# Optimization experiments

Measured on AMD Instinct MI355X. Metric: run time of the kernel, lower is better.

Reference implementation:

```python
import jax, jax.numpy as jnp
import numpy as np
import math

D_MODEL = 512
NHEAD = 8
HEAD_DIM = D_MODEL // NHEAD
LN_EPS = 1e-5


def _layernorm(x, g, b):
    mu = jnp.mean(x, axis=-1, keepdims=True)
    var = jnp.mean(jnp.square(x - mu), axis=-1, keepdims=True)
    return (x - mu) * jax.lax.rsqrt(var + LN_EPS) * g + b


def setup_inputs() -> dict:
    key = jax.random.key(0)
    ks = jax.random.split(key, 12)
    B, N, D = 4, 2048, D_MODEL
    s = 1.0 / math.sqrt(D)
    inp = {
        "hidden": jax.random.normal(ks[0], (B, N, D), jnp.float32),
        "adjacency": (jax.random.uniform(ks[1], (B, N, N)) > 0.98).astype(jnp.float32),
        "Wq": jax.random.normal(ks[2], (D, D), jnp.float32) * s,
        "bq": jnp.zeros((D,), jnp.float32),
        "Wk": jax.random.normal(ks[3], (D, D), jnp.float32) * s,
        "bk": jnp.zeros((D,), jnp.float32),
        "Wv": jax.random.normal(ks[4], (D, D), jnp.float32) * s,
        "bv": jnp.zeros((D,), jnp.float32),
        "Wo": jax.random.normal(ks[5], (D, D), jnp.float32) * s,
        "bo": jnp.zeros((D,), jnp.float32),
        "g1": jnp.ones((D,), jnp.float32),
        "b1": jnp.zeros((D,), jnp.float32),
        "g2": jnp.ones((D,), jnp.float32),
        "b2": jnp.zeros((D,), jnp.float32),
        "Wf1": jax.random.normal(ks[6], (D, 4 * D), jnp.float32) * s,
        "bf1": jnp.zeros((4 * D,), jnp.float32),
        "Wf2": jax.random.normal(ks[7], (4 * D, D), jnp.float32) * (1.0 / math.sqrt(4 * D)),
        "bf2": jnp.zeros((D,), jnp.float32),
    }
    return inp


def reference(hidden, adjacency, Wq, bq, Wk, bk, Wv, bv, Wo, bo,
              g1, b1, g2, b2, Wf1, bf1, Wf2, bf2):
    B, N, D = hidden.shape
    H, Hd = NHEAD, HEAD_DIM
    normed = _layernorm(hidden, g1, b1)
    # projections -> [B, H, N, Hd]
    q = (normed @ Wq + bq).reshape(B, N, H, Hd).transpose(0, 2, 1, 3)
    k = (normed @ Wk + bk).reshape(B, N, H, Hd).transpose(0, 2, 1, 3)
    v = (normed @ Wv + bv).reshape(B, N, H, Hd).transpose(0, 2, 1, 3)
    logits = jnp.einsum('bhnd,bhmd->bhnm', q, k) / math.sqrt(Hd)
    adj = adjacency[:, None, :, :]            # [B, 1, N, N]
    logits = logits + (2.0 * adj - 1.0)       # conditioned bias
    weights = jax.nn.softmax(logits, axis=-1)
    weights = weights * (0.25 + 0.75 * adj)   # post-softmax renorm
    weights = weights / jnp.maximum(weights.sum(axis=-1, keepdims=True), 1e-6)
    attended = jnp.einsum('bhnm,bhmd->bhnd', weights, v)
    attended = attended.transpose(0, 2, 1, 3).reshape(B, N, D)
    hidden = hidden + attended @ Wo + bo
    h2 = _layernorm(hidden, g2, b2)
    ff = jax.nn.gelu(h2 @ Wf1 + bf1, approximate=False) @ Wf2 + bf2
    return hidden + ff
```

## Files before the change

kernel.cpp:

```cpp
#include <hip/hip_runtime.h>
#include <stdint.h>

typedef unsigned short u16;
typedef unsigned long long u64;
typedef __bf16 bf16x8 __attribute__((ext_vector_type(8)));
typedef float f32x4 __attribute__((ext_vector_type(4)));
typedef float f32x16 __attribute__((ext_vector_type(16)));
typedef u16 u16x8 __attribute__((ext_vector_type(8)));

__device__ __forceinline__ u16 f2bf(float x) {
    union { float f; uint32_t u; } c; c.f = x;
    uint32_t r = (c.u + 0x7fffu + ((c.u >> 16) & 1u)) >> 16;
    return (u16)r;
}
__device__ __forceinline__ float bf2f(u16 x) {
    union { uint32_t u; float f; } c; c.u = ((uint32_t)x) << 16;
    return c.f;
}

__device__ __forceinline__ void async16(const void* g, void* l) {
    __builtin_amdgcn_global_load_lds(
        (const __attribute__((address_space(1))) uint32_t*)g,
        (__attribute__((address_space(3))) uint32_t*)l,
        16, 0, 0);
}

__device__ __forceinline__ void permswap(uint32_t& a, uint32_t& b) {
    asm volatile("v_permlane32_swap_b32 %0, %1" : "+v"(a), "+v"(b));
}

__global__ void transpose_all(const float* __restrict__ Wq, const float* __restrict__ Wk,
                              const float* __restrict__ Wv, const float* __restrict__ Wo,
                              const float* __restrict__ Wf1, const float* __restrict__ Wf2,
                              u16* __restrict__ wqkv, u16* __restrict__ wo,
                              u16* __restrict__ wf1, u16* __restrict__ wf2) {
    __shared__ float t[64][65];
    int bid = blockIdx.x;
    const float* src; u16* dst; int K, N, lb;
    if (bid < 256) {
        K = 512; N = 512;
        int which = bid >> 6; lb = bid & 63;
        src = which == 0 ? Wq : (which == 1 ? Wk : (which == 2 ? Wv : Wo));
        dst = which == 3 ? wo : wqkv + (size_t)which * 512 * 512;
    } else if (bid < 512) {
        K = 512; N = 2048; lb = bid - 256; src = Wf1; dst = wf1;
    } else {
        K = 2048; N = 512; lb = bid - 512; src = Wf2; dst = wf2;
    }
    const int nt = N / 64;
    const int k0 = (lb / nt) * 64, n0 = (lb % nt) * 64;
    const int c = threadIdx.x & 63, r0 = threadIdx.x >> 6;
#pragma unroll
    for (int i = 0; i < 16; ++i) {
        int r = r0 + i * 4;
        t[r][c] = src[(size_t)(k0 + r) * N + n0 + c];
    }
    __syncthreads();
#pragma unroll
    for (int i = 0; i < 16; ++i) {
        int r = r0 + i * 4;
        dst[(size_t)(n0 + r) * K + k0 + c] = f2bf(t[c][r]);
    }
}

__global__ void transpose_v(const u16* __restrict__ src, u16* __restrict__ dst) {
    __shared__ u16 t[64][66];
    const int bh = blockIdx.x >> 5, kt = blockIdx.x & 31;
    const int tid = threadIdx.x;
    const u16* sp = src + ((size_t)bh * 2048 + kt * 64) * 64;
#pragma unroll
    for (int i = 0; i < 2; ++i) {
        int r = (tid >> 3) + i * 32;
        int c0 = (tid & 7) * 8;
        u16x8 v = *(const u16x8*)(sp + (size_t)r * 64 + c0);
#pragma unroll
        for (int j = 0; j < 8; ++j) t[r][c0 + j] = v[j];
    }
    __syncthreads();
    u16* dp = dst + ((size_t)bh * 64) * 2048 + kt * 64;
#pragma unroll
    for (int i = 0; i < 2; ++i) {
        int d = (tid >> 3) + i * 32;
        int k0 = (tid & 7) * 8;
        u16x8 o;
#pragma unroll
        for (int j = 0; j < 8; ++j) o[j] = t[k0 + j][d];
        *(u16x8*)(dp + (size_t)d * 2048 + k0) = o;
    }
}

__global__ void pack_adj(const float* __restrict__ adj, u64* __restrict__ bits) {
    const int wid = blockIdx.x * 4 + (threadIdx.x >> 6);
    const int lane = threadIdx.x & 63;
    float v = adj[(size_t)wid * 64 + lane];
    u64 mask = __ballot(v > 0.5f);
    if (lane == 0) bits[wid] = mask;
}

template <int BFIN>
__global__ void ln_kernel(const void* __restrict__ xv, const float* __restrict__ g,
                          const float* __restrict__ b, u16* __restrict__ out) {
    const int w = threadIdx.x >> 6, lane = threadIdx.x & 63;
    const int row = blockIdx.x * 4 + w;
    float f[8];
    if constexpr (BFIN) {
        const u16* xr = (const u16*)xv + (size_t)row * 512 + lane * 8;
        u16x8 v = *(const u16x8*)xr;
#pragma unroll
        for (int j = 0; j < 8; ++j) f[j] = bf2f(v[j]);
    } else {
        const float* xr = (const float*)xv + (size_t)row * 512 + lane * 8;
        float4 v0 = *(const float4*)xr;
        float4 v1 = *(const float4*)(xr + 4);
        f[0] = v0.x; f[1] = v0.y; f[2] = v0.z; f[3] = v0.w;
        f[4] = v1.x; f[5] = v1.y; f[6] = v1.z; f[7] = v1.w;
    }
    float sum = 0.f, sq = 0.f;
#pragma unroll
    for (int j = 0; j < 8; ++j) { sum += f[j]; sq += f[j] * f[j]; }
#pragma unroll
    for (int m = 1; m < 64; m <<= 1) {
        sum += __shfl_xor(sum, m);
        sq  += __shfl_xor(sq, m);
    }
    float mu = sum * (1.f / 512.f);
    float var = sq * (1.f / 512.f) - mu * mu;
    float rs = rsqrtf(var + 1e-5f);
    float4 g0 = *(const float4*)(g + lane * 8), g1 = *(const float4*)(g + lane * 8 + 4);
    float4 b0 = *(const float4*)(b + lane * 8), b1 = *(const float4*)(b + lane * 8 + 4);
    float gg[8] = {g0.x, g0.y, g0.z, g0.w, g1.x, g1.y, g1.z, g1.w};
    float bb[8] = {b0.x, b0.y, b0.z, b0.w, b1.x, b1.y, b1.z, b1.w};
    u16x8 o;
#pragma unroll
    for (int j = 0; j < 8; ++j) o[j] = f2bf((f[j] - mu) * rs * gg[j] + bb[j]);
    *(u16x8*)(out + (size_t)row * 512 + lane * 8) = o;
}

template <int WM, int WN, int EPI, int MINW>
__global__ __launch_bounds__(256, MINW)
void gemm_bt(const u16* __restrict__ A, const u16* __restrict__ Bt,
             int N, int K,
             const float* __restrict__ b0, const float* __restrict__ b1,
             const float* __restrict__ b2, const float* __restrict__ addf,
             const u16* __restrict__ addbf, float* __restrict__ outf,
             u16* __restrict__ o0, u16* __restrict__ o1, u16* __restrict__ o2) {
    constexpr int BM = 2 * WM, BN = 2 * WN;
    constexpr int MI = WM / 16, NI = WN / 16;
    constexpr int LA = BM / 32, LB = BN / 32;
    __shared__ __align__(16) u16 Als[BM * 64];
    __shared__ __align__(16) u16 Bls[BN * 64];
    const int tid = threadIdx.x, w = tid >> 6, lane = tid & 63;
    const int bid = ((int)blockIdx.x & 7) * ((int)gridDim.x >> 3) + ((int)blockIdx.x >> 3);
    const int nbn = N / BN;
    const int bm0 = (bid / nbn) * BM;
    const int bn0 = (bid % nbn) * BN;
    const int wr = w >> 1, wc = w & 1;
    const int srow = lane >> 3, schunk = lane & 7;
    f32x4 acc[MI][NI];
#pragma unroll
    for (int i = 0; i < MI; ++i)
#pragma unroll
        for (int j = 0; j < NI; ++j) acc[i][j] = f32x4{0.f, 0.f, 0.f, 0.f};

    for (int k0 = 0; k0 < K; k0 += 64) {
#pragma unroll
        for (int j = 0; j < LA; ++j) {
            int li = w * LA + j;
            int r = li * 8 + srow;
            async16(A + (size_t)(bm0 + r) * K + k0 + ((schunk ^ (r & 7)) << 3), &Als[li * 512]);
        }
#pragma unroll
        for (int j = 0; j < LB; ++j) {
            int li = w * LB + j;
            int r = li * 8 + srow;
            async16(Bt + (size_t)(bn0 + r) * K + k0 + ((schunk ^ (r & 7)) << 3), &Bls[li * 512]);
        }
        __syncthreads();
#pragma unroll
        for (int ks = 0; ks < 2; ++ks) {
            bf16x8 af[MI], bfr[NI];
            const int ck = ks * 4 + (lane >> 4);
#pragma unroll
            for (int mi = 0; mi < MI; ++mi) {
                int r = wr * WM + mi * 16 + (lane & 15);
                af[mi] = *(const bf16x8*)&Als[r * 64 + ((ck ^ (r & 7)) << 3)];
            }
#pragma unroll
            for (int ni = 0; ni < NI; ++ni) {
                int r = wc * WN + ni * 16 + (lane & 15);
                bfr[ni] = *(const bf16x8*)&Bls[r * 64 + ((ck ^ (r & 7)) << 3)];
            }
#pragma unroll
            for (int mi = 0; mi < MI; ++mi)
#pragma unroll
                for (int ni = 0; ni < NI; ++ni)
                    acc[mi][ni] = __builtin_amdgcn_mfma_f32_16x16x32_bf16(
                        af[mi], bfr[ni], acc[mi][ni], 0, 0, 0);
        }
        __syncthreads();
    }
#pragma unroll
    for (int mi = 0; mi < MI; ++mi)
#pragma unroll
        for (int ni = 0; ni < NI; ++ni)
#pragma unroll
            for (int reg = 0; reg < 4; ++reg) {
                int row = bm0 + wr * WM + mi * 16 + ((lane >> 4) << 2) + reg;
                int col = bn0 + wc * WN + ni * 16 + (lane & 15);
                float val = acc[mi][ni][reg];
                if constexpr (EPI == 0) {
                    int wsel = col >> 9, jj = col & 511;
                    const float* bb = wsel == 0 ? b0 : (wsel == 1 ? b1 : b2);
                    u16* dst = wsel == 0 ? o0 : (wsel == 1 ? o1 : o2);
                    val += bb[jj];
                    int h = jj >> 6, hd = jj & 63;
                    int b_ = row >> 11, n_ = row & 2047;
                    dst[(((size_t)(b_ * 8 + h) * 2048 + n_) << 6) + hd] = f2bf(val);
                } else if constexpr (EPI == 1) {
                    val += b0[col] + addf[(size_t)row * 512 + col];
                    o0[(size_t)row * 512 + col] = f2bf(val);
                } else if constexpr (EPI == 2) {
                    float x = val + b0[col];
                    float gx = 0.5f * x * (1.0f + erff(x * 0.70710678118654752f));
                    o0[(size_t)row * 2048 + col] = f2bf(gx);
                } else {
                    val += b0[col] + bf2f(addbf[(size_t)row * 512 + col]);
                    outf[(size_t)row * 512 + col] = val;
                }
            }
}

__global__ __launch_bounds__(256, 3)
void attn32_kernel(const u16* __restrict__ q, const u16* __restrict__ k,
                   const u16* __restrict__ vT, const u64* __restrict__ adjbits,
                   u16* __restrict__ att) {
    const int tid = threadIdx.x, w = tid >> 6;
    const int lane = tid & 63, col = lane & 31, g = lane >> 5;
    const int qg = w >> 1, ks = w & 1;
    const int bh = blockIdx.x & 31, qt = blockIdx.x >> 5;
    const int b_ = bh >> 3, h_ = bh & 7;
    __shared__ __align__(16) u16 Vt[2][2][4096];
    __shared__ float Lls[2][2][32];
    const int q0 = qt * 64 + qg * 32;
    const int myq = q0 + col;
    const u16* qptr = q + ((size_t)bh * 2048 + myq) * 64 + g * 8;
    const u16* kptr = k + ((size_t)bh * 2048 + ks * 1024 + col) * 64 + g * 8;
    const u64* adjrow = adjbits + ((size_t)b_ * 2048 + myq) * 32 + ks * 16;
    const int sr = lane >> 3, sc = lane & 7;
    const u16* vstage = vT + ((size_t)bh * 64 + qg * 32 + sr) * 2048 + ks * 1024 +
                        ((sc ^ sr) << 3);

    bf16x8 Qf[4];
#pragma unroll
    for (int c = 0; c < 4; ++c) Qf[c] = *(const bf16x8*)(qptr + c * 16);
    f32x16 O0, O1;
#pragma unroll
    for (int i = 0; i < 16; ++i) { O0[i] = 0.f; O1[i] = 0.f; }
    float L = 0.f;

    auto stage = [&](int it, int buf) {
#pragma unroll
        for (int j = 0; j < 4; ++j)
            async16(vstage + (size_t)j * 8 * 2048 + it * 64,
                    &Vt[ks][buf][(qg * 4 + j) * 512]);
    };
    stage(0, 0);
    __syncthreads();

    for (int it = 0; it < 16; ++it) {
        const int cur = it & 1;
        if (it < 15) stage(it + 1, cur ^ 1);
        const u64 adjw = adjrow[it];
        const char* vt = (const char*)&Vt[ks][cur][0];
#pragma unroll
        for (int s = 0; s < 2; ++s) {
            bf16x8 Ku[4];
#pragma unroll
            for (int c = 0; c < 4; ++c)
                Ku[c] = *(const bf16x8*)(kptr + (size_t)(it * 64 + s * 32) * 64 + c * 16);
            f32x16 S;
#pragma unroll
            for (int i = 0; i < 16; ++i) S[i] = 0.f;
            __builtin_amdgcn_s_setprio(1);
#pragma unroll
            for (int c = 0; c < 4; ++c)
                S = __builtin_amdgcn_mfma_f32_32x32x16_bf16(Ku[c], Qf[c], S, 0, 0, 0);
            __builtin_amdgcn_s_setprio(0);
            uint32_t w32 = (uint32_t)(adjw >> (32 * s));
            float p[16];
#pragma unroll
            for (int r_ = 0; r_ < 16; ++r_) {
                int bit = (r_ & 3) + 8 * (r_ >> 2) + 4 * g;
                float cst = ((w32 >> bit) & 1u) ? -15.8696454f : -20.7550354f;
                p[r_] = __builtin_amdgcn_exp2f(S[r_] * 0.18033688f + cst);
            }
            float t0 = (p[0] + p[1]) + (p[2] + p[3]);
            float t1 = (p[4] + p[5]) + (p[6] + p[7]);
            float t2s = (p[8] + p[9]) + (p[10] + p[11]);
            float t3 = (p[12] + p[13]) + (p[14] + p[15]);
            L += (t0 + t1) + (t2s + t3);
            uint32_t pk[8];
#pragma unroll
            for (int i = 0; i < 8; ++i) {
                union { __bf16 h[2]; uint32_t u; } pu;
                pu.h[0] = (__bf16)p[2 * i]; pu.h[1] = (__bf16)p[2 * i + 1];
                pk[i] = pu.u;
            }
            permswap(pk[0], pk[2]); permswap(pk[1], pk[3]);
            permswap(pk[4], pk[6]); permswap(pk[5], pk[7]);
            union { uint32_t u[4]; bf16x8 v; } fa0, fa1;
            fa0.u[0] = pk[0]; fa0.u[1] = pk[1]; fa0.u[2] = pk[2]; fa0.u[3] = pk[3];
            fa1.u[0] = pk[4]; fa1.u[1] = pk[5]; fa1.u[2] = pk[6]; fa1.u[3] = pk[7];
            __builtin_amdgcn_s_setprio(1);
#pragma unroll
            for (int c2 = 0; c2 < 2; ++c2) {
                int kb = (s * 32 + c2 * 16 + g * 8) * 2;
                int r0 = col, r1 = 32 + col;
                bf16x8 fv0 = *(const bf16x8*)(vt + ((r0 * 128 + kb) ^ ((r0 & 7) << 4)));
                bf16x8 fv1 = *(const bf16x8*)(vt + ((r1 * 128 + kb) ^ ((r1 & 7) << 4)));
                const bf16x8 fa = c2 ? fa1.v : fa0.v;
                O0 = __builtin_amdgcn_mfma_f32_32x32x16_bf16(fa, fv0, O0, 0, 0, 0);
                O1 = __builtin_amdgcn_mfma_f32_32x32x16_bf16(fa, fv1, O1, 0, 0, 0);
            }
            __builtin_amdgcn_s_setprio(0);
        }
        __syncthreads();
    }

    float Lt = L + __shfl_xor(L, 32);
    if (g == 0) Lls[qg][ks][col] = Lt;
    __syncthreads();
    float* Obuf = (float*)&Vt[0][0][0];
    if (ks == 1) {
#pragma unroll
        for (int r_ = 0; r_ < 16; ++r_) {
            int qrow = (r_ & 3) + 8 * (r_ >> 2) + 4 * g;
            Obuf[((qg * 32 + qrow) << 6) + col] = O0[r_];
            Obuf[((qg * 32 + qrow) << 6) + 32 + col] = O1[r_];
        }
    }
    __syncthreads();
    if (ks == 0) {
        u16* outp = att + ((size_t)b_ * 2048 + q0) * 512 + (h_ << 6);
#pragma unroll
        for (int r_ = 0; r_ < 16; ++r_) {
            int qrow = (r_ & 3) + 8 * (r_ >> 2) + 4 * g;
            float lsum = Lls[qg][0][qrow] + Lls[qg][1][qrow];
            float inv = __builtin_amdgcn_rcpf(lsum);
            float o0 = O0[r_] + Obuf[((qg * 32 + qrow) << 6) + col];
            float o1 = O1[r_] + Obuf[((qg * 32 + qrow) << 6) + 32 + col];
            outp[(size_t)qrow * 512 + col] = f2bf(o0 * inv);
            outp[(size_t)qrow * 512 + 32 + col] = f2bf(o1 * inv);
        }
    }
}

extern "C" void kernel_launch(void* const* d_in, const int* in_sizes, int n_in,
                              void* d_out, int out_size, void* d_ws, size_t ws_size,
                              hipStream_t stream) {
    const float* hidden = (const float*)d_in[0];
    const float* adj    = (const float*)d_in[1];
    const float* Wq = (const float*)d_in[2];
    const float* bq = (const float*)d_in[3];
    const float* Wk = (const float*)d_in[4];
    const float* bk = (const float*)d_in[5];
    const float* Wv = (const float*)d_in[6];
    const float* bv = (const float*)d_in[7];
    const float* Wo = (const float*)d_in[8];
    const float* bo = (const float*)d_in[9];
    const float* g1 = (const float*)d_in[10];
    const float* b1 = (const float*)d_in[11];
    const float* g2 = (const float*)d_in[12];
    const float* b2 = (const float*)d_in[13];
    const float* Wf1 = (const float*)d_in[14];
    const float* bf1 = (const float*)d_in[15];
    const float* Wf2 = (const float*)d_in[16];
    const float* bf2 = (const float*)d_in[17];
    float* out = (float*)d_out;

    char* p = (char*)d_ws;
    u16* wqkv_t = (u16*)p; p += (size_t)1536 * 512 * 2;
    u16* wo_t   = (u16*)p; p += (size_t)512 * 512 * 2;
    u16* wf1_t  = (u16*)p; p += (size_t)2048 * 512 * 2;
    u16* wf2_t  = (u16*)p; p += (size_t)512 * 2048 * 2;
    u64* adjbits = (u64*)p; p += (size_t)4 * 2048 * 32 * 8;
    u16* bufA = (u16*)p; p += (size_t)8192 * 512 * 2;
    u16* bufQ = (u16*)p; p += (size_t)8192 * 512 * 2;
    float* midreg = (float*)p; p += (size_t)8192 * 512 * 4;
    u16* kbuf = (u16*)p; p += (size_t)8192 * 512 * 2;
    u16* vbuf = (u16*)p; p += (size_t)8192 * 512 * 2;
    p += (size_t)16 * 1024 * 1024;
    u16* ffh = kbuf;
    u16* vT  = (u16*)midreg;
    u16* mid = (u16*)midreg + (size_t)8192 * 512;
    (void)ws_size; (void)in_sizes; (void)n_in; (void)out_size;

    transpose_all<<<768, 256, 0, stream>>>(Wq, Wk, Wv, Wo, Wf1, Wf2,
                                           wqkv_t, wo_t, wf1_t, wf2_t);
    pack_adj<<<65536, 256, 0, stream>>>(adj, adjbits);
    ln_kernel<0><<<2048, 256, 0, stream>>>(hidden, g1, b1, bufA);
    gemm_bt<64, 64, 0, 3><<<64 * 12, 256, 0, stream>>>(bufA, wqkv_t, 1536, 512,
        bq, bk, bv, nullptr, nullptr, nullptr, bufQ, kbuf, vbuf);
    transpose_v<<<1024, 256, 0, stream>>>(vbuf, vT);
    attn32_kernel<<<1024, 256, 0, stream>>>(bufQ, kbuf, vT, adjbits, bufA);
    gemm_bt<32, 64, 1, 4><<<512, 256, 0, stream>>>(bufA, wo_t, 512, 512,
        bo, nullptr, nullptr, hidden, nullptr, nullptr, mid, nullptr, nullptr);
    ln_kernel<1><<<2048, 256, 0, stream>>>(mid, g2, b2, bufQ);
    gemm_bt<64, 64, 2, 3><<<64 * 16, 256, 0, stream>>>(bufQ, wf1_t, 2048, 512,
        bf1, nullptr, nullptr, nullptr, nullptr, nullptr, ffh, nullptr, nullptr);
    gemm_bt<32, 64, 3, 4><<<512, 256, 0, stream>>>(ffh, wf2_t, 512, 2048,
        bf2, nullptr, nullptr, nullptr, mid, out, nullptr, nullptr, nullptr);
}
```

Measured before the change: 229.8 us.

## Fuse V transpose into QKV epilogue and rewrite attention with 16x16 MFMA tiles

The QKV GEMM epilogue now writes V directly in transposed [bh, hd, n] layout, so the separate transpose_v launch goes away. The attention kernel is rewritten from 32x32x16 MFMA tiles with permlane swaps to 16x16x32 QK tiles and 16x16x16 PV tiles, using fewer registers so occupancy can rise from 3 to 4 blocks. The transposed V write in the epilogue is a strided scatter that may coalesce poorly. The smaller MFMA shapes mean more instructions are issued per tile.

```diff
diff --git a/kernel.cpp b/kernel.cpp
--- a/kernel.cpp
+++ b/kernel.cpp
@@ -4,8 +4,8 @@
 typedef unsigned short u16;
 typedef unsigned long long u64;
 typedef __bf16 bf16x8 __attribute__((ext_vector_type(8)));
+typedef __bf16 bf16x4 __attribute__((ext_vector_type(4)));
 typedef float f32x4 __attribute__((ext_vector_type(4)));
-typedef float f32x16 __attribute__((ext_vector_type(16)));
 typedef u16 u16x8 __attribute__((ext_vector_type(8)));
 
 __device__ __forceinline__ u16 f2bf(float x) {
@@ -25,8 +25,18 @@
         16, 0, 0);
 }
 
-__device__ __forceinline__ void permswap(uint32_t& a, uint32_t& b) {
-    asm volatile("v_permlane32_swap_b32 %0, %1" : "+v"(a), "+v"(b));
+__device__ __forceinline__ f32x4 pv_mfma(bf16x4 a, bf16x4 b, f32x4 c) {
+#if __has_builtin(__builtin_amdgcn_mfma_f32_16x16x16_bf16)
+    return __builtin_amdgcn_mfma_f32_16x16x16_bf16(a, b, c, 0, 0, 0);
+#elif __has_builtin(__builtin_amdgcn_mfma_f32_16x16x16bf16_1k)
+    typedef short s16x4 __attribute__((ext_vector_type(4)));
+    union { bf16x4 h; s16x4 s; } ua, ub; ua.h = a; ub.h = b;
+    return __builtin_amdgcn_mfma_f32_16x16x16bf16_1k(ua.s, ub.s, c, 0, 0, 0);
+#else
+    f32x4 d = c;
+    asm("v_mfma_f32_16x16x16_bf16 %0, %1, %2, %0" : "+v"(d) : "v"(a), "v"(b));
+    return d;
+#endif
 }
 
 __global__ void transpose_all(const float* __restrict__ Wq, const float* __restrict__ Wk,
@@ -60,32 +70,6 @@
     for (int i = 0; i < 16; ++i) {
         int r = r0 + i * 4;
         dst[(size_t)(n0 + r) * K + k0 + c] = f2bf(t[c][r]);
-    }
-}
-
-__global__ void transpose_v(const u16* __restrict__ src, u16* __restrict__ dst) {
-    __shared__ u16 t[64][66];
-    const int bh = blockIdx.x >> 5, kt = blockIdx.x & 31;
-    const int tid = threadIdx.x;
-    const u16* sp = src + ((size_t)bh * 2048 + kt * 64) * 64;
-#pragma unroll
-    for (int i = 0; i < 2; ++i) {
-        int r = (tid >> 3) + i * 32;
-        int c0 = (tid & 7) * 8;
-        u16x8 v = *(const u16x8*)(sp + (size_t)r * 64 + c0);
-#pragma unroll
-        for (int j = 0; j < 8; ++j) t[r][c0 + j] = v[j];
-    }
-    __syncthreads();
-    u16* dp = dst + ((size_t)bh * 64) * 2048 + kt * 64;
-#pragma unroll
-    for (int i = 0; i < 2; ++i) {
-        int d = (tid >> 3) + i * 32;
-        int k0 = (tid & 7) * 8;
-        u16x8 o;
-#pragma unroll
-        for (int j = 0; j < 8; ++j) o[j] = t[k0 + j][d];
-        *(u16x8*)(dp + (size_t)d * 2048 + k0) = o;
     }
 }
 
@@ -211,11 +195,15 @@
                 if constexpr (EPI == 0) {
                     int wsel = col >> 9, jj = col & 511;
                     const float* bb = wsel == 0 ? b0 : (wsel == 1 ? b1 : b2);
-                    u16* dst = wsel == 0 ? o0 : (wsel == 1 ? o1 : o2);
                     val += bb[jj];
                     int h = jj >> 6, hd = jj & 63;
                     int b_ = row >> 11, n_ = row & 2047;
-                    dst[(((size_t)(b_ * 8 + h) * 2048 + n_) << 6) + hd] = f2bf(val);
+                    if (wsel == 2) {
+                        o2[(((size_t)(b_ * 8 + h) * 64 + hd) << 11) + n_] = f2bf(val);
+                    } else {
+                        u16* dst = wsel == 0 ? o0 : o1;
+                        dst[(((size_t)(b_ * 8 + h) * 2048 + n_) << 6) + hd] = f2bf(val);
+                    }
                 } else if constexpr (EPI == 1) {
                     val += b0[col] + addf[(size_t)row * 512 + col];
                     o0[(size_t)row * 512 + col] = f2bf(val);
@@ -230,33 +218,36 @@
             }
 }
 
-__global__ __launch_bounds__(256, 3)
-void attn32_kernel(const u16* __restrict__ q, const u16* __restrict__ k,
+__global__ __launch_bounds__(256, 4)
+void attn16_kernel(const u16* __restrict__ q, const u16* __restrict__ k,
                    const u16* __restrict__ vT, const u64* __restrict__ adjbits,
                    u16* __restrict__ att) {
     const int tid = threadIdx.x, w = tid >> 6;
-    const int lane = tid & 63, col = lane & 31, g = lane >> 5;
+    const int lane = tid & 63, l15 = lane & 15, g4 = lane >> 4;
     const int qg = w >> 1, ks = w & 1;
     const int bh = blockIdx.x & 31, qt = blockIdx.x >> 5;
     const int b_ = bh >> 3, h_ = bh & 7;
     __shared__ __align__(16) u16 Vt[2][2][4096];
     __shared__ float Lls[2][2][32];
     const int q0 = qt * 64 + qg * 32;
-    const int myq = q0 + col;
-    const u16* qptr = q + ((size_t)bh * 2048 + myq) * 64 + g * 8;
-    const u16* kptr = k + ((size_t)bh * 2048 + ks * 1024 + col) * 64 + g * 8;
-    const u64* adjrow = adjbits + ((size_t)b_ * 2048 + myq) * 32 + ks * 16;
+    const u16* kbase = k + ((size_t)bh * 2048 + ks * 1024 + l15) * 64 + g4 * 8;
+    const u64* adjr0 = adjbits + ((size_t)b_ * 2048 + q0 + l15) * 32 + ks * 16;
+    const u64* adjr1 = adjr0 + 16 * 32;
     const int sr = lane >> 3, sc = lane & 7;
     const u16* vstage = vT + ((size_t)bh * 64 + qg * 32 + sr) * 2048 + ks * 1024 +
                         ((sc ^ sr) << 3);
 
-    bf16x8 Qf[4];
-#pragma unroll
-    for (int c = 0; c < 4; ++c) Qf[c] = *(const bf16x8*)(qptr + c * 16);
-    f32x16 O0, O1;
-#pragma unroll
-    for (int i = 0; i < 16; ++i) { O0[i] = 0.f; O1[i] = 0.f; }
-    float L = 0.f;
+    bf16x8 Qf[2][2];
+#pragma unroll
+    for (int qt2 = 0; qt2 < 2; ++qt2)
+#pragma unroll
+        for (int c = 0; c < 2; ++c)
+            Qf[qt2][c] = *(const bf16x8*)(q + ((size_t)bh * 2048 + q0 + qt2 * 16 + l15) * 64
+                                          + c * 32 + g4 * 8);
+    f32x4 O0[4], O1[4];
+#pragma unroll
+    for (int t = 0; t < 4; ++t) { O0[t] = f32x4{0.f,0.f,0.f,0.f}; O1[t] = f32x4{0.f,0.f,0.f,0.f}; }
+    float L0 = 0.f, L1 = 0.f;
 
     auto stage = [&](int it, int buf) {
 #pragma unroll
@@ -267,91 +258,90 @@
     stage(0, 0);
     __syncthreads();
 
+    const int vx = l15 & 7;
     for (int it = 0; it < 16; ++it) {
         const int cur = it & 1;
         if (it < 15) stage(it + 1, cur ^ 1);
-        const u64 adjw = adjrow[it];
+        const u64 a0 = adjr0[it] >> (g4 * 4);
+        const u64 a1 = adjr1[it] >> (g4 * 4);
         const char* vt = (const char*)&Vt[ks][cur][0];
 #pragma unroll
-        for (int s = 0; s < 2; ++s) {
-            bf16x8 Ku[4];
-#pragma unroll
-            for (int c = 0; c < 4; ++c)
-                Ku[c] = *(const bf16x8*)(kptr + (size_t)(it * 64 + s * 32) * 64 + c * 16);
-            f32x16 S;
-#pragma unroll
-            for (int i = 0; i < 16; ++i) S[i] = 0.f;
+        for (int st = 0; st < 4; ++st) {
+            bf16x8 Ka0 = *(const bf16x8*)(kbase + (size_t)(it * 64 + st * 16) * 64);
+            bf16x8 Ka1 = *(const bf16x8*)(kbase + (size_t)(it * 64 + st * 16) * 64 + 32);
+            f32x4 S0 = f32x4{0.f,0.f,0.f,0.f}, S1 = f32x4{0.f,0.f,0.f,0.f};
             __builtin_amdgcn_s_setprio(1);
-#pragma unroll
-            for (int c = 0; c < 4; ++c)
-                S = __builtin_amdgcn_mfma_f32_32x32x16_bf16(Ku[c], Qf[c], S, 0, 0, 0);
+            S0 = __builtin_amdgcn_mfma_f32_16x16x32_bf16(Ka0, Qf[0][0], S0, 0, 0, 0);
+            S0 = __builtin_amdgcn_mfma_f32_16x16x32_bf16(Ka1, Qf[0][1], S0, 0, 0, 0);
+            S1 = __builtin_amdgcn_mfma_f32_16x16x32_bf16(Ka0, Qf[1][0], S1, 0, 0, 0);
+            S1 = __builtin_amdgcn_mfma_f32_16x16x32_bf16(Ka1, Qf[1][1], S1, 0, 0, 0);
             __builtin_amdgcn_s_setprio(0);
-            uint32_t w32 = (uint32_t)(adjw >> (32 * s));
-            float p[16];
-#pragma unroll
-            for (int r_ = 0; r_ < 16; ++r_) {
-                int bit = (r_ & 3) + 8 * (r_ >> 2) + 4 * g;
-                float cst = ((w32 >> bit) & 1u) ? -15.8696454f : -20.7550354f;
-                p[r_] = __builtin_amdgcn_exp2f(S[r_] * 0.18033688f + cst);
+            float p0[4], p1[4];
+#pragma unroll
+            for (int r_ = 0; r_ < 4; ++r_) {
+                uint32_t e0 = (uint32_t)(a0 >> (st * 16 + r_)) & 1u;
+                uint32_t e1 = (uint32_t)(a1 >> (st * 16 + r_)) & 1u;
+                float c0 = e0 ? -15.8696454f : -20.7550354f;
+                float c1 = e1 ? -15.8696454f : -20.7550354f;
+                p0[r_] = __builtin_amdgcn_exp2f(S0[r_] * 0.18033688f + c0);
+                p1[r_] = __builtin_amdgcn_exp2f(S1[r_] * 0.18033688f + c1);
             }
-            float t0 = (p[0] + p[1]) + (p[2] + p[3]);
-            float t1 = (p[4] + p[5]) + (p[6] + p[7]);
-            float t2s = (p[8] + p[9]) + (p[10] + p[11]);
-            float t3 = (p[12] + p[13]) + (p[14] + p[15]);
-            L += (t0 + t1) + (t2s + t3);
-            uint32_t pk[8];
-#pragma unroll
-            for (int i = 0; i < 8; ++i) {
-                union { __bf16 h[2]; uint32_t u; } pu;
-                pu.h[0] = (__bf16)p[2 * i]; pu.h[1] = (__bf16)p[2 * i + 1];
-                pk[i] = pu.u;
-            }
-            permswap(pk[0], pk[2]); permswap(pk[1], pk[3]);
-            permswap(pk[4], pk[6]); permswap(pk[5], pk[7]);
-            union { uint32_t u[4]; bf16x8 v; } fa0, fa1;
-            fa0.u[0] = pk[0]; fa0.u[1] = pk[1]; fa0.u[2] = pk[2]; fa0.u[3] = pk[3];
-            fa1.u[0] = pk[4]; fa1.u[1] = pk[5]; fa1.u[2] = pk[6]; fa1.u[3] = pk[7];
+            L0 += (p0[0] + p0[1]) + (p0[2] + p0[3]);
+            L1 += (p1[0] + p1[1]) + (p1[2] + p1[3]);
+            bf16x4 pa0 = {(__bf16)p0[0], (__bf16)p0[1], (__bf16)p0[2], (__bf16)p0[3]};
+            bf16x4 pa1 = {(__bf16)p1[0], (__bf16)p1[1], (__bf16)p1[2], (__bf16)p1[3]};
             __builtin_amdgcn_s_setprio(1);
 #pragma unroll
-            for (int c2 = 0; c2 < 2; ++c2) {
-                int kb = (s * 32 + c2 * 16 + g * 8) * 2;
-                int r0 = col, r1 = 32 + col;
-                bf16x8 fv0 = *(const bf16x8*)(vt + ((r0 * 128 + kb) ^ ((r0 & 7) << 4)));
-                bf16x8 fv1 = *(const bf16x8*)(vt + ((r1 * 128 + kb) ^ ((r1 & 7) << 4)));
-                const bf16x8 fa = c2 ? fa1.v : fa0.v;
-                O0 = __builtin_amdgcn_mfma_f32_32x32x16_bf16(fa, fv0, O0, 0, 0, 0);
-                O1 = __builtin_amdgcn_mfma_f32_32x32x16_bf16(fa, fv1, O1, 0, 0, 0);
+            for (int t = 0; t < 4; ++t) {
+                int row = t * 16 + l15;
+                int chunk = (st * 2 + (g4 >> 1)) ^ vx;
+                bf16x4 bv = *(const bf16x4*)(vt + row * 128 + chunk * 16 + (g4 & 1) * 8);
+                O0[t] = pv_mfma(pa0, bv, O0[t]);
+                O1[t] = pv_mfma(pa1, bv, O1[t]);
             }
             __builtin_amdgcn_s_setprio(0);
         }
         __syncthreads();
     }
 
-    float Lt = L + __shfl_xor(L, 32);
-    if (g == 0) Lls[qg][ks][col] = Lt;
+    float Lt0 = L0 + __shfl_xor(L0, 16); Lt0 += __shfl_xor(Lt0, 32);
+    float Lt1 = L1 + __shfl_xor(L1, 16); Lt1 += __shfl_xor(Lt1, 32);
+    if (g4 == 0) {
+        Lls[qg][ks][l15] = Lt0;
+        Lls[qg][ks][16 + l15] = Lt1;
+    }
     __syncthreads();
     float* Obuf = (float*)&Vt[0][0][0];
     if (ks == 1) {
 #pragma unroll
-        for (int r_ = 0; r_ < 16; ++r_) {
-            int qrow = (r_ & 3) + 8 * (r_ >> 2) + 4 * g;
-            Obuf[((qg * 32 + qrow) << 6) + col] = O0[r_];
-            Obuf[((qg * 32 + qrow) << 6) + 32 + col] = O1[r_];
-        }
+        for (int qt2 = 0; qt2 < 2; ++qt2)
+#pragma unroll
+            for (int t = 0; t < 4; ++t)
+#pragma unroll
+                for (int r_ = 0; r_ < 4; ++r_) {
+                    int qloc = qt2 * 16 + g4 * 4 + r_;
+                    int hd = t * 16 + l15;
+                    float v = qt2 ? O1[t][r_] : O0[t][r_];
+                    Obuf[((qg * 32 + qloc) << 6) + hd] = v;
+                }
     }
     __syncthreads();
     if (ks == 0) {
         u16* outp = att + ((size_t)b_ * 2048 + q0) * 512 + (h_ << 6);
 #pragma unroll
-        for (int r_ = 0; r_ < 16; ++r_) {
-            int qrow = (r_ & 3) + 8 * (r_ >> 2) + 4 * g;
-            float lsum = Lls[qg][0][qrow] + Lls[qg][1][qrow];
-            float inv = __builtin_amdgcn_rcpf(lsum);
-            float o0 = O0[r_] + Obuf[((qg * 32 + qrow) << 6) + col];
-            float o1 = O1[r_] + Obuf[((qg * 32 + qrow) << 6) + 32 + col];
-            outp[(size_t)qrow * 512 + col] = f2bf(o0 * inv);
-            outp[(size_t)qrow * 512 + 32 + col] = f2bf(o1 * inv);
-        }
+        for (int qt2 = 0; qt2 < 2; ++qt2)
+#pragma unroll
+            for (int t = 0; t < 4; ++t)
+#pragma unroll
+                for (int r_ = 0; r_ < 4; ++r_) {
+                    int qloc = qt2 * 16 + g4 * 4 + r_;
+                    int hd = t * 16 + l15;
+                    float lsum = Lls[qg][0][qloc] + Lls[qg][1][qloc];
+                    float inv = __builtin_amdgcn_rcpf(lsum);
+                    float v = (qt2 ? O1[t][r_] : O0[t][r_]) +
+                              Obuf[((qg * 32 + qloc) << 6) + hd];
+                    outp[(size_t)qloc * 512 + hd] = f2bf(v * inv);
+                }
     }
 }
 
@@ -393,16 +383,15 @@
     u16* ffh = kbuf;
     u16* vT  = (u16*)midreg;
     u16* mid = (u16*)midreg + (size_t)8192 * 512;
-    (void)ws_size; (void)in_sizes; (void)n_in; (void)out_size;
+    (void)vbuf; (void)ws_size; (void)in_sizes; (void)n_in; (void)out_size;
 
     transpose_all<<<768, 256, 0, stream>>>(Wq, Wk, Wv, Wo, Wf1, Wf2,
                                            wqkv_t, wo_t, wf1_t, wf2_t);
     pack_adj<<<65536, 256, 0, stream>>>(adj, adjbits);
     ln_kernel<0><<<2048, 256, 0, stream>>>(hidden, g1, b1, bufA);
     gemm_bt<64, 64, 0, 3><<<64 * 12, 256, 0, stream>>>(bufA, wqkv_t, 1536, 512,
-        bq, bk, bv, nullptr, nullptr, nullptr, bufQ, kbuf, vbuf);
-    transpose_v<<<1024, 256, 0, stream>>>(vbuf, vT);
-    attn32_kernel<<<1024, 256, 0, stream>>>(bufQ, kbuf, vT, adjbits, bufA);
+        bq, bk, bv, nullptr, nullptr, nullptr, bufQ, kbuf, vT);
+    attn16_kernel<<<1024, 256, 0, stream>>>(bufQ, kbuf, vT, adjbits, bufA);
     gemm_bt<32, 64, 1, 4><<<512, 256, 0, stream>>>(bufA, wo_t, 512, 512,
         bo, nullptr, nullptr, hidden, nullptr, nullptr, mid, nullptr, nullptr);
     ln_kernel<1><<<2048, 256, 0, stream>>>(mid, g2, b2, bufQ);
```

Result: slower. 271.8 us (+18.3%).

## Merge weight transpose, adjacency packing and first LayerNorm into one prep kernel

Applied to the files above, without the earlier changes.

Three independent preprocessing kernels (weight transpose/convert, adjacency bit packing, first LayerNorm) are combined into a single launch whose blocks branch by block index. The adjacency packing also changes from one ballot per wave per block of 65536 blocks to each wave handling 32 words with four ballots in flight, cutting block count and adding memory-level parallelism. This removes two launch gaps and lets the independent work overlap on the device, at the cost of a larger kernel with mixed block roles.

```diff
diff --git a/kernel.cpp b/kernel.cpp
--- a/kernel.cpp
+++ b/kernel.cpp
@@ -29,37 +29,83 @@
     asm volatile("v_permlane32_swap_b32 %0, %1" : "+v"(a), "+v"(b));
 }
 
-__global__ void transpose_all(const float* __restrict__ Wq, const float* __restrict__ Wk,
-                              const float* __restrict__ Wv, const float* __restrict__ Wo,
-                              const float* __restrict__ Wf1, const float* __restrict__ Wf2,
-                              u16* __restrict__ wqkv, u16* __restrict__ wo,
-                              u16* __restrict__ wf1, u16* __restrict__ wf2) {
+__global__ void prep_kernel(const float* __restrict__ Wq, const float* __restrict__ Wk,
+                            const float* __restrict__ Wv, const float* __restrict__ Wo,
+                            const float* __restrict__ Wf1, const float* __restrict__ Wf2,
+                            const float* __restrict__ adj, const float* __restrict__ hidden,
+                            const float* __restrict__ g1, const float* __restrict__ b1,
+                            u16* __restrict__ wqkv, u16* __restrict__ wo,
+                            u16* __restrict__ wf1, u16* __restrict__ wf2,
+                            u64* __restrict__ bits, u16* __restrict__ ln1out) {
     __shared__ float t[64][65];
-    int bid = blockIdx.x;
-    const float* src; u16* dst; int K, N, lb;
-    if (bid < 256) {
-        K = 512; N = 512;
-        int which = bid >> 6; lb = bid & 63;
-        src = which == 0 ? Wq : (which == 1 ? Wk : (which == 2 ? Wv : Wo));
-        dst = which == 3 ? wo : wqkv + (size_t)which * 512 * 512;
-    } else if (bid < 512) {
-        K = 512; N = 2048; lb = bid - 256; src = Wf1; dst = wf1;
+    const int bid = blockIdx.x, tid = threadIdx.x;
+    if (bid < 768) {
+        const float* src; u16* dst; int K, N, lb;
+        if (bid < 256) {
+            K = 512; N = 512;
+            int which = bid >> 6; lb = bid & 63;
+            src = which == 0 ? Wq : (which == 1 ? Wk : (which == 2 ? Wv : Wo));
+            dst = which == 3 ? wo : wqkv + (size_t)which * 512 * 512;
+        } else if (bid < 512) {
+            K = 512; N = 2048; lb = bid - 256; src = Wf1; dst = wf1;
+        } else {
+            K = 2048; N = 512; lb = bid - 512; src = Wf2; dst = wf2;
+        }
+        const int nt = N / 64;
+        const int k0 = (lb / nt) * 64, n0 = (lb % nt) * 64;
+        const int c = tid & 63, r0 = tid >> 6;
+#pragma unroll
+        for (int i = 0; i < 16; ++i) {
+            int r = r0 + i * 4;
+            t[r][c] = src[(size_t)(k0 + r) * N + n0 + c];
+        }
+        __syncthreads();
+#pragma unroll
+        for (int i = 0; i < 16; ++i) {
+            int r = r0 + i * 4;
+            dst[(size_t)(n0 + r) * K + k0 + c] = f2bf(t[c][r]);
+        }
+    } else if (bid < 2816) {
+        const int wv = (bid - 768) * 4 + (tid >> 6), lane = tid & 63;
+        const size_t wbase = (size_t)wv * 32;
+#pragma unroll
+        for (int s = 0; s < 8; ++s) {
+            size_t w0 = wbase + s * 4;
+            const float* fp = adj + w0 * 64 + lane;
+            u64 m0 = __ballot(fp[0]   > 0.5f);
+            u64 m1 = __ballot(fp[64]  > 0.5f);
+            u64 m2 = __ballot(fp[128] > 0.5f);
+            u64 m3 = __ballot(fp[192] > 0.5f);
+            if (lane == 0) {
+                bits[w0] = m0; bits[w0 + 1] = m1; bits[w0 + 2] = m2; bits[w0 + 3] = m3;
+            }
+        }
     } else {
-        K = 2048; N = 512; lb = bid - 512; src = Wf2; dst = wf2;
-    }
-    const int nt = N / 64;
-    const int k0 = (lb / nt) * 64, n0 = (lb % nt) * 64;
-    const int c = threadIdx.x & 63, r0 = threadIdx.x >> 6;
-#pragma unroll
-    for (int i = 0; i < 16; ++i) {
-        int r = r0 + i * 4;
-        t[r][c] = src[(size_t)(k0 + r) * N + n0 + c];
-    }
-    __syncthreads();
-#pragma unroll
-    for (int i = 0; i < 16; ++i) {
-        int r = r0 + i * 4;
-        dst[(size_t)(n0 + r) * K + k0 + c] = f2bf(t[c][r]);
+        const int w = tid >> 6, lane = tid & 63;
+        const int row = (bid - 2816) * 4 + w;
+        const float* xr = hidden + (size_t)row * 512 + lane * 8;
+        float4 v0 = *(const float4*)xr;
+        float4 v1 = *(const float4*)(xr + 4);
+        float f[8] = {v0.x, v0.y, v0.z, v0.w, v1.x, v1.y, v1.z, v1.w};
+        float sum = 0.f, sq = 0.f;
+#pragma unroll
+        for (int j = 0; j < 8; ++j) { sum += f[j]; sq += f[j] * f[j]; }
+#pragma unroll
+        for (int m = 1; m < 64; m <<= 1) {
+            sum += __shfl_xor(sum, m);
+            sq  += __shfl_xor(sq, m);
+        }
+        float mu = sum * (1.f / 512.f);
+        float var = sq * (1.f / 512.f) - mu * mu;
+        float rs = rsqrtf(var + 1e-5f);
+        float4 g0 = *(const float4*)(g1 + lane * 8), gg1 = *(const float4*)(g1 + lane * 8 + 4);
+        float4 bb0 = *(const float4*)(b1 + lane * 8), bb1 = *(const float4*)(b1 + lane * 8 + 4);
+        float gg[8] = {g0.x, g0.y, g0.z, g0.w, gg1.x, gg1.y, gg1.z, gg1.w};
+        float bb[8] = {bb0.x, bb0.y, bb0.z, bb0.w, bb1.x, bb1.y, bb1.z, bb1.w};
+        u16x8 o;
+#pragma unroll
+        for (int j = 0; j < 8; ++j) o[j] = f2bf((f[j] - mu) * rs * gg[j] + bb[j]);
+        *(u16x8*)(ln1out + (size_t)row * 512 + lane * 8) = o;
     }
 }
 
@@ -89,32 +135,15 @@
     }
 }
 
-__global__ void pack_adj(const float* __restrict__ adj, u64* __restrict__ bits) {
-    const int wid = blockIdx.x * 4 + (threadIdx.x >> 6);
-    const int lane = threadIdx.x & 63;
-    float v = adj[(size_t)wid * 64 + lane];
-    u64 mask = __ballot(v > 0.5f);
-    if (lane == 0) bits[wid] = mask;
-}
-
-template <int BFIN>
-__global__ void ln_kernel(const void* __restrict__ xv, const float* __restrict__ g,
-                          const float* __restrict__ b, u16* __restrict__ out) {
+__global__ void ln2_kernel(const u16* __restrict__ x, const float* __restrict__ g,
+                           const float* __restrict__ b, u16* __restrict__ out) {
     const int w = threadIdx.x >> 6, lane = threadIdx.x & 63;
     const int row = blockIdx.x * 4 + w;
+    const u16* xr = x + (size_t)row * 512 + lane * 8;
+    u16x8 v = *(const u16x8*)xr;
     float f[8];
-    if constexpr (BFIN) {
-        const u16* xr = (const u16*)xv + (size_t)row * 512 + lane * 8;
-        u16x8 v = *(const u16x8*)xr;
-#pragma unroll
-        for (int j = 0; j < 8; ++j) f[j] = bf2f(v[j]);
-    } else {
-        const float* xr = (const float*)xv + (size_t)row * 512 + lane * 8;
-        float4 v0 = *(const float4*)xr;
-        float4 v1 = *(const float4*)(xr + 4);
-        f[0] = v0.x; f[1] = v0.y; f[2] = v0.z; f[3] = v0.w;
-        f[4] = v1.x; f[5] = v1.y; f[6] = v1.z; f[7] = v1.w;
-    }
+#pragma unroll
+    for (int j = 0; j < 8; ++j) f[j] = bf2f(v[j]);
     float sum = 0.f, sq = 0.f;
 #pragma unroll
     for (int j = 0; j < 8; ++j) { sum += f[j]; sq += f[j] * f[j]; }
@@ -395,17 +424,16 @@
     u16* mid = (u16*)midreg + (size_t)8192 * 512;
     (void)ws_size; (void)in_sizes; (void)n_in; (void)out_size;
 
-    transpose_all<<<768, 256, 0, stream>>>(Wq, Wk, Wv, Wo, Wf1, Wf2,
-                                           wqkv_t, wo_t, wf1_t, wf2_t);
-    pack_adj<<<65536, 256, 0, stream>>>(adj, adjbits);
-    ln_kernel<0><<<2048, 256, 0, stream>>>(hidden, g1, b1, bufA);
+    prep_kernel<<<4864, 256, 0, stream>>>(Wq, Wk, Wv, Wo, Wf1, Wf2, adj, hidden,
+                                          g1, b1, wqkv_t, wo_t, wf1_t, wf2_t,
+                                          adjbits, bufA);
     gemm_bt<64, 64, 0, 3><<<64 * 12, 256, 0, stream>>>(bufA, wqkv_t, 1536, 512,
         bq, bk, bv, nullptr, nullptr, nullptr, bufQ, kbuf, vbuf);
     transpose_v<<<1024, 256, 0, stream>>>(vbuf, vT);
     attn32_kernel<<<1024, 256, 0, stream>>>(bufQ, kbuf, vT, adjbits, bufA);
     gemm_bt<32, 64, 1, 4><<<512, 256, 0, stream>>>(bufA, wo_t, 512, 512,
         bo, nullptr, nullptr, hidden, nullptr, nullptr, mid, nullptr, nullptr);
-    ln_kernel<1><<<2048, 256, 0, stream>>>(mid, g2, b2, bufQ);
+    ln2_kernel<<<2048, 256, 0, stream>>>(mid, g2, b2, bufQ);
     gemm_bt<64, 64, 2, 3><<<64 * 16, 256, 0, stream>>>(bufQ, wf1_t, 2048, 512,
         bf1, nullptr, nullptr, nullptr, nullptr, nullptr, ffh, nullptr, nullptr);
     gemm_bt<32, 64, 3, 4><<<512, 256, 0, stream>>>(ffh, wf2_t, 512, 2048,
```

Result: faster. 211.0 us, median of 2 (-8.2%).
